# Performance work log

Hardware: AMD Instinct MI355X
Metric: run time of the kernel (lower is better)

## Reference

```python
import jax, jax.numpy as jnp
import numpy as np

HIDDEN = 1024
N_HEADS = 16
HEAD_DIM = HIDDEN // N_HEADS  # 64
SCALE = HEAD_DIM ** -0.5
B, QL, KVL = 2, 2048, 4096


def setup_inputs() -> dict:
    key = jax.random.key(0)
    ks = jax.random.split(key, 7)
    s = 0.02
    return {
        "query_states": jax.random.normal(ks[0], (B, QL, HIDDEN), jnp.float32),
        "key_states": jax.random.normal(ks[1], (B, KVL, HIDDEN), jnp.float32),
        "value_states": jax.random.normal(ks[2], (B, KVL, HIDDEN), jnp.float32),
        # torch nn.Linear weights: shape [out, in], applied as x @ W.T
        "Wq": jax.random.normal(ks[3], (HIDDEN, HIDDEN), jnp.float32) * s,
        "Wk": jax.random.normal(ks[4], (HIDDEN, HIDDEN), jnp.float32) * s,
        "Wv": jax.random.normal(ks[5], (HIDDEN, HIDDEN), jnp.float32) * s,
        "Wo": jax.random.normal(ks[6], (HIDDEN, HIDDEN), jnp.float32) * s,
    }


def reference(query_states, key_states, value_states, Wq, Wk, Wv, Wo):
    b, ql, _ = query_states.shape
    kvl = key_states.shape[1]
    # projections (torch Linear: x @ W.T)
    q = query_states @ Wq.T  # [b, ql, H]
    k = key_states @ Wk.T    # [b, kvl, H]
    v = value_states @ Wv.T  # [b, kvl, H]
    # split heads -> [b, h, s, d]
    q = q.reshape(b, ql, N_HEADS, HEAD_DIM).transpose(0, 2, 1, 3)
    k = k.reshape(b, kvl, N_HEADS, HEAD_DIM).transpose(0, 2, 1, 3)
    v = v.reshape(b, kvl, N_HEADS, HEAD_DIM).transpose(0, 2, 1, 3)
    # scores [b, h, ql, kvl]
    scores = jnp.einsum("bhqd,bhkd->bhqk", q, k) * SCALE
    attn = jax.nn.softmax(scores, axis=-1)
    out = jnp.einsum("bhqk,bhkd->bhqd", attn, v)  # [b, h, ql, d]
    out = out.transpose(0, 2, 1, 3).reshape(b, ql, HIDDEN)
    return out @ Wo.T
```

## Files before the change

### kernel.cpp

```cpp
#include <hip/hip_runtime.h>

#define HID   1024
#define NH    16
#define HD    64
#define QL    2048
#define KVL   4096
#define NB    2
#define QSCALE 0.180336880111120426f

typedef short s8v  __attribute__((ext_vector_type(8)));
typedef short s4v  __attribute__((ext_vector_type(4)));
typedef float f4v  __attribute__((ext_vector_type(4)));

__device__ __forceinline__ unsigned short f2bf(float f) {
  unsigned int u = __builtin_bit_cast(unsigned int, f);
  u += 0x7FFFu + ((u >> 16) & 1u);
  return (unsigned short)(u >> 16);
}
__device__ __forceinline__ float bf2f(unsigned short h) {
  unsigned int u = ((unsigned int)h) << 16;
  return __builtin_bit_cast(float, u);
}
__device__ __forceinline__ float fexp2(float x) {
#if __has_builtin(__builtin_amdgcn_exp2f)
  return __builtin_amdgcn_exp2f(x);
#else
  return exp2f(x);
#endif
}

__global__ __launch_bounds__(256)
void cast_all(const float* __restrict__ q, const float* __restrict__ k,
              const float* __restrict__ v, const float* __restrict__ wq,
              const float* __restrict__ wk, const float* __restrict__ wv,
              const float* __restrict__ wo, unsigned short* __restrict__ dst) {
  size_t c = (size_t)blockIdx.x * 256 + threadIdx.x;
  const float* src; size_t lc; float sc = 1.0f;
  if (c < 524288)       { src = q;  lc = c; }
  else if (c < 1572864) { src = k;  lc = c - 524288; }
  else if (c < 2621440) { src = v;  lc = c - 1572864; }
  else if (c < 2752512) { src = wq; lc = c - 2621440; sc = QSCALE; }
  else if (c < 2883584) { src = wk; lc = c - 2752512; }
  else if (c < 3014656) { src = wv; lc = c - 2883584; }
  else                  { src = wo; lc = c - 3014656; }
  const float4* p = (const float4*)(src + lc * 8);
  float4 a = p[0], b = p[1];
  union { s8v v8; unsigned short h[8]; } u;
  u.h[0] = f2bf(a.x * sc); u.h[1] = f2bf(a.y * sc);
  u.h[2] = f2bf(a.z * sc); u.h[3] = f2bf(a.w * sc);
  u.h[4] = f2bf(b.x * sc); u.h[5] = f2bf(b.y * sc);
  u.h[6] = f2bf(b.z * sc); u.h[7] = f2bf(b.w * sc);
  *(s8v*)(dst + c * 8) = u.v8;
}

typedef const __attribute__((address_space(1))) unsigned int* gas_t;
typedef __attribute__((address_space(3))) unsigned int*       las_t;

__device__ __forceinline__ void gl_lds16(const unsigned short* g, unsigned short* l) {
  __builtin_amdgcn_global_load_lds((gas_t)(const void*)g, (las_t)(void*)l, 16, 0, 0);
}

template <bool OUT_BF16>
__device__ __forceinline__ void gemm_body(const unsigned short* __restrict__ A,
                                          const unsigned short* __restrict__ B,
                                          void* __restrict__ Cv, int N, int K,
                                          int bx, int by,
                                          unsigned short (*As)[128 * 32],
                                          unsigned short (*Bs)[128 * 32]) {
  const int tid  = threadIdx.x;
  const int wave = tid >> 6, lane = tid & 63;
  const int wm = wave >> 1, wn = wave & 1;
  const int quad = lane >> 4, l15 = lane & 15;
  const int row0 = by * 128;
  const int col0 = bx * 128;
  const int srow = lane >> 2;
  const int scol = (lane & 3) * 8;

  f4v acc[4][4] = {};

#define G_STAGE(KI, BI)                                                         \
  {                                                                             \
    _Pragma("unroll")                                                           \
    for (int cc = 0; cc < 2; cc++) {                                            \
      int c = wave + cc * 4;                                                    \
      gl_lds16(A + (size_t)(row0 + c * 16 + srow) * K + (KI) * 32 + scol,       \
               &As[BI][c * 512]);                                               \
      gl_lds16(B + (size_t)(col0 + c * 16 + srow) * K + (KI) * 32 + scol,       \
               &Bs[BI][c * 512]);                                               \
    }                                                                           \
  }

  const int nk = K >> 5;
  G_STAGE(0, 0);
  __syncthreads();

  for (int ki = 0; ki < nk; ki++) {
    const int cur = ki & 1;
    if (ki + 1 < nk) G_STAGE(ki + 1, 1 - cur);

    s8v af[4], bf[4];
#pragma unroll
    for (int i = 0; i < 4; i++)
      af[i] = *(const s8v*)&As[cur][(wm * 64 + i * 16 + l15) * 32 + quad * 8];
#pragma unroll
    for (int j = 0; j < 4; j++)
      bf[j] = *(const s8v*)&Bs[cur][(wn * 64 + j * 16 + l15) * 32 + quad * 8];
#pragma unroll
    for (int i = 0; i < 4; i++)
#pragma unroll
      for (int j = 0; j < 4; j++)
        acc[i][j] = __builtin_amdgcn_mfma_f32_16x16x32_bf16(af[i], bf[j],
                                                            acc[i][j], 0, 0, 0);
    __syncthreads();
  }
#undef G_STAGE

#pragma unroll
  for (int i = 0; i < 4; i++) {
#pragma unroll
    for (int j = 0; j < 4; j++) {
      int r = row0 + wm * 64 + i * 16 + quad * 4;
      int c = col0 + wn * 64 + j * 16 + l15;
#pragma unroll
      for (int reg = 0; reg < 4; reg++) {
        float v = acc[i][j][reg];
        if constexpr (OUT_BF16)
          ((unsigned short*)Cv)[(size_t)(r + reg) * N + c] = f2bf(v);
        else
          ((float*)Cv)[(size_t)(r + reg) * N + c] = v;
      }
    }
  }
}

__global__ __launch_bounds__(256, 4)
void proj_fused(const unsigned short* __restrict__ qc, const unsigned short* __restrict__ kc,
                const unsigned short* __restrict__ vc, const unsigned short* __restrict__ wqc,
                const unsigned short* __restrict__ wkc, const unsigned short* __restrict__ wvc,
                unsigned short* __restrict__ qp, unsigned short* __restrict__ kp,
                unsigned short* __restrict__ vpt) {
  __shared__ unsigned short As[2][128 * 32];
  __shared__ unsigned short Bs[2][128 * 32];
  int bid = blockIdx.x;
  if (bid < 256) {
    gemm_body<true>(qc, wqc, qp, HID, HID, bid & 7, bid >> 3, As, Bs);
  } else if (bid < 768) {
    int l = bid - 256;
    gemm_body<true>(kc, wkc, kp, HID, HID, l & 7, l >> 3, As, Bs);
  } else {
    int l = bid - 768;
    int b = l >> 8, r = l & 255;
    gemm_body<true>(wvc, vc + (size_t)b * KVL * HID,
                    vpt + (size_t)b * HID * KVL, KVL, HID, r & 31, r >> 5, As, Bs);
  }
}

__global__ __launch_bounds__(256, 4)
void o_gemm(const unsigned short* __restrict__ ao, const unsigned short* __restrict__ woc,
            float* __restrict__ out) {
  __shared__ unsigned short As[2][128 * 32];
  __shared__ unsigned short Bs[2][128 * 32];
  int bid = blockIdx.x;
  gemm_body<false>(ao, woc, out, HID, HID, bid & 7, bid >> 3, As, Bs);
}

#define LDSK 40

template <typename T>
__device__ __forceinline__ void stage_tile(unsigned short* dst, const T* src,
                                           int ld, int tid, float sc) {
#pragma unroll
  for (int rep = 0; rep < 2; rep++) {
    int s = rep * 256 + tid;
    int row = s >> 2;
    int cs  = (s & 3) * 8;
    const T* p = src + (size_t)row * ld + cs;
    s8v val;
    if constexpr (sizeof(T) == 4) {
      float4 f0 = *(const float4*)p;
      float4 f1 = *(const float4*)(p + 4);
      union { s8v v; unsigned short h[8]; } u;
      u.h[0] = f2bf(f0.x * sc); u.h[1] = f2bf(f0.y * sc);
      u.h[2] = f2bf(f0.z * sc); u.h[3] = f2bf(f0.w * sc);
      u.h[4] = f2bf(f1.x * sc); u.h[5] = f2bf(f1.y * sc);
      u.h[6] = f2bf(f1.z * sc); u.h[7] = f2bf(f1.w * sc);
      val = u.v;
    } else {
      val = *(const s8v*)p;
    }
    *(s8v*)&dst[row * LDSK + cs] = val;
  }
}

template <typename TA, typename TB, bool OUT_BF16>
__global__ __launch_bounds__(256)
void gemm_conv(const TA* __restrict__ A, const TB* __restrict__ B,
               void* __restrict__ Cv, int M, int N, int K, float bscale,
               long long bz, long long cz) {
  __shared__ unsigned short As[128 * LDSK];
  __shared__ unsigned short Bs[128 * LDSK];
  const TB* Bp = B + (size_t)blockIdx.z * (size_t)bz;
  const int tid  = threadIdx.x;
  const int wave = tid >> 6, lane = tid & 63;
  const int wm = wave >> 1, wn = wave & 1;
  const int quad = lane >> 4, l15 = lane & 15;
  const int row0 = blockIdx.y * 128;
  const int col0 = blockIdx.x * 128;

  f4v acc[4][4] = {};

  for (int k0 = 0; k0 < K; k0 += 32) {
    __syncthreads();
    stage_tile(As, A + (size_t)row0 * K + k0, K, tid, 1.0f);
    stage_tile(Bs, Bp + (size_t)col0 * K + k0, K, tid, bscale);
    __syncthreads();

    s8v af[4], bf[4];
#pragma unroll
    for (int i = 0; i < 4; i++)
      af[i] = *(const s8v*)&As[(wm * 64 + i * 16 + l15) * LDSK + quad * 8];
#pragma unroll
    for (int j = 0; j < 4; j++)
      bf[j] = *(const s8v*)&Bs[(wn * 64 + j * 16 + l15) * LDSK + quad * 8];
#pragma unroll
    for (int i = 0; i < 4; i++)
#pragma unroll
      for (int j = 0; j < 4; j++)
        acc[i][j] = __builtin_amdgcn_mfma_f32_16x16x32_bf16(af[i], bf[j],
                                                            acc[i][j], 0, 0, 0);
  }

  char* Cp = (char*)Cv + (size_t)blockIdx.z * (size_t)cz * (OUT_BF16 ? 2 : 4);
#pragma unroll
  for (int i = 0; i < 4; i++) {
#pragma unroll
    for (int j = 0; j < 4; j++) {
      int r = row0 + wm * 64 + i * 16 + quad * 4;
      int c = col0 + wn * 64 + j * 16 + l15;
#pragma unroll
      for (int reg = 0; reg < 4; reg++) {
        float v = acc[i][j][reg];
        if constexpr (OUT_BF16)
          ((unsigned short*)Cp)[(size_t)(r + reg) * N + c] = f2bf(v);
        else
          ((float*)Cp)[(size_t)(r + reg) * N + c] = v;
      }
    }
  }
}

template <bool SPLIT>
__global__ __launch_bounds__(256, 2)
void attn6(const unsigned short* __restrict__ qp,
           const unsigned short* __restrict__ kp,
           const unsigned short* __restrict__ vpt,
           unsigned short* __restrict__ po,
           float* __restrict__ pl,
           unsigned short* __restrict__ ao) {
  __shared__ unsigned short Ks[2][64 * 64];
  __shared__ unsigned short Vt[2][64 * 64];
  __shared__ unsigned short Pt[4][64 * 64];

  const int bid  = blockIdx.x;
  const int qb   = bid & 7;
  const int h    = (bid >> 3) & 15;
  const int b    = (bid >> 7) & 1;
  const int half = SPLIT ? (bid >> 8) : 0;
  const int tid  = threadIdx.x;
  const int wave = tid >> 6, lane = tid & 63;
  const int quad = lane >> 4, l15 = lane & 15;
  const int q0   = qb * 256 + wave * 64;
  const int kvoff = half * (KVL / 2);
  const int NT   = SPLIT ? (KVL / 128) : (KVL / 64);

  const unsigned short* kbase = kp + (size_t)b * KVL * HID + h * HD + (size_t)kvoff * HID;
  const unsigned short* vbase = vpt + (size_t)(b * NH + h) * HD * KVL + kvoff;

  int prow[2], pcol[2], pbase[2];
#pragma unroll
  for (int i = 0; i < 2; i++) {
    int p = (i * 4 + wave) * 64 + lane;
    prow[i]  = p >> 3;
    pcol[i]  = ((p & 7) ^ (prow[i] & 7)) * 8;
    pbase[i] = (i * 4 + wave) * 512;
  }

  s8v qf[4][2];
#pragma unroll
  for (int nt = 0; nt < 4; nt++) {
    const size_t qrow = (size_t)(b * QL + q0 + nt * 16 + l15) * HID + h * HD;
#pragma unroll
    for (int ks = 0; ks < 2; ks++)
      qf[nt][ks] = *(const s8v*)(qp + qrow + ks * 32 + quad * 8);
  }

  float lrun[4] = {0.f, 0.f, 0.f, 0.f};
  f4v oacc[4][4] = {};

#define STAGE_KV(KT, BI)                                                        \
  {                                                                             \
    const unsigned short* kb = kbase + (size_t)((KT) * 64) * HID;               \
    const unsigned short* vb = vbase + (KT) * 64;                               \
    _Pragma("unroll")                                                           \
    for (int i = 0; i < 2; i++) {                                               \
      gl_lds16(kb + (size_t)prow[i] * HID + pcol[i], &Ks[BI][pbase[i]]);        \
      gl_lds16(vb + (size_t)prow[i] * KVL + pcol[i], &Vt[BI][pbase[i]]);        \
    }                                                                           \
  }

  STAGE_KV(0, 0);
  __syncthreads();

  for (int kt = 0; kt < NT; kt++) {
    const int cur = kt & 1;
    if (kt + 1 < NT) STAGE_KV(kt + 1, 1 - cur);

    f4v sacc[4][4] = {};
#pragma unroll
    for (int ks = 0; ks < 2; ks++)
#pragma unroll
      for (int mt = 0; mt < 4; mt++) {
        int row = mt * 16 + l15;
        int xc  = ((ks * 4 + quad) ^ (row & 7)) * 8;
        s8v kf = *(const s8v*)&Ks[cur][row * 64 + xc];
#pragma unroll
        for (int nt = 0; nt < 4; nt++)
          sacc[mt][nt] = __builtin_amdgcn_mfma_f32_16x16x32_bf16(kf, qf[nt][ks],
                                                                 sacc[mt][nt], 0, 0, 0);
      }

#pragma unroll
    for (int nt = 0; nt < 4; nt++) {
      float rs = 0.f;
#pragma unroll
      for (int mt = 0; mt < 4; mt++) {
        float p0 = fexp2(sacc[mt][nt][0]);
        float p1 = fexp2(sacc[mt][nt][1]);
        float p2 = fexp2(sacc[mt][nt][2]);
        float p3 = fexp2(sacc[mt][nt][3]);
        rs += (p0 + p1) + (p2 + p3);
        union { s4v v4; unsigned short hh[4]; } pk;
        pk.hh[0] = (unsigned short)(__builtin_bit_cast(unsigned int, p0) >> 16);
        pk.hh[1] = (unsigned short)(__builtin_bit_cast(unsigned int, p1) >> 16);
        pk.hh[2] = (unsigned short)(__builtin_bit_cast(unsigned int, p2) >> 16);
        pk.hh[3] = (unsigned short)(__builtin_bit_cast(unsigned int, p3) >> 16);
        int row = nt * 16 + l15;
        int c   = mt * 2 + (quad >> 1);
        int off = ((c ^ (row & 7)) * 8) + (quad & 1) * 4;
        *(s4v*)&Pt[wave][row * 64 + off] = pk.v4;
      }
      rs += __shfl_xor(rs, 16, 64);
      rs += __shfl_xor(rs, 32, 64);
      lrun[nt] += rs;
    }

#pragma unroll
    for (int ch = 0; ch < 2; ch++) {
      s8v vf[4];
#pragma unroll
      for (int dt = 0; dt < 4; dt++) {
        int row = dt * 16 + l15;
        int xc  = ((ch * 4 + quad) ^ (row & 7)) * 8;
        vf[dt] = *(const s8v*)&Vt[cur][row * 64 + xc];
      }
#pragma unroll
      for (int qt = 0; qt < 4; qt++) {
        int row = qt * 16 + l15;
        int xc  = ((ch * 4 + quad) ^ (row & 7)) * 8;
        s8v pf = *(const s8v*)&Pt[wave][row * 64 + xc];
#pragma unroll
        for (int dt = 0; dt < 4; dt++)
          oacc[qt][dt] = __builtin_amdgcn_mfma_f32_16x16x32_bf16(pf, vf[dt],
                                                                 oacc[qt][dt], 0, 0, 0);
      }
    }

    __syncthreads();
  }
#undef STAGE_KV

  if constexpr (SPLIT) {
    unsigned short* pob = po + (size_t)half * NB * QL * HID;
#pragma unroll
    for (int qt = 0; qt < 4; qt++) {
#pragma unroll
      for (int dt = 0; dt < 4; dt++)
#pragma unroll
        for (int r = 0; r < 4; r++) {
          int qq = q0 + qt * 16 + quad * 4 + r;
          int cc = h * HD + dt * 16 + l15;
          pob[(size_t)(b * QL + qq) * HID + cc] = f2bf(oacc[qt][dt][r]);
        }
      if (quad == 0)
        pl[(size_t)half * NB * NH * QL + (b * NH + h) * QL + q0 + qt * 16 + l15] = lrun[qt];
    }
  } else {
#pragma unroll
    for (int qt = 0; qt < 4; qt++) {
      float li = 1.0f / lrun[qt];
      float lr[4];
#pragma unroll
      for (int r = 0; r < 4; r++)
        lr[r] = __shfl(li, (lane & 48) + quad * 4 + r, 64);
#pragma unroll
      for (int dt = 0; dt < 4; dt++)
#pragma unroll
        for (int r = 0; r < 4; r++) {
          int qq = q0 + qt * 16 + quad * 4 + r;
          int cc = h * HD + dt * 16 + l15;
          ao[(size_t)(b * QL + qq) * HID + cc] = f2bf(oacc[qt][dt][r] * lr[r]);
        }
    }
  }
}

__global__ __launch_bounds__(256)
void combine(const unsigned short* __restrict__ po, const float* __restrict__ pl,
             unsigned short* __restrict__ ao) {
  int t  = blockIdx.x * 256 + threadIdx.x;
  int r  = t >> 7;
  int c8 = t & 127;
  int b = r >> 11, q = r & 2047, h = c8 >> 3;
  size_t lidx = (size_t)(b * NH + h) * QL + q;
  float l = pl[lidx] + pl[(size_t)NB * NH * QL + lidx];
  float inv = 1.0f / l;
  size_t off = (size_t)r * HID + c8 * 8;
  s8v a = *(const s8v*)(po + off);
  s8v c = *(const s8v*)(po + (size_t)NB * QL * HID + off);
  union { s8v v8; unsigned short hh[8]; } ua, uc, uo;
  ua.v8 = a; uc.v8 = c;
#pragma unroll
  for (int e = 0; e < 8; e++)
    uo.hh[e] = f2bf((bf2f(ua.hh[e]) + bf2f(uc.hh[e])) * inv);
  *(s8v*)(ao + off) = uo.v8;
}

extern "C" void kernel_launch(void* const* d_in, const int* in_sizes, int n_in,
                              void* d_out, int out_size, void* d_ws, size_t ws_size,
                              hipStream_t stream) {
  const float* q  = (const float*)d_in[0];
  const float* k  = (const float*)d_in[1];
  const float* v  = (const float*)d_in[2];
  const float* Wq = (const float*)d_in[3];
  const float* Wk = (const float*)d_in[4];
  const float* Wv = (const float*)d_in[5];
  const float* Wo = (const float*)d_in[6];
  float* out = (float*)d_out;
  char* ws = (char*)d_ws;
  dim3 blk(256);

  const long long MB = 1024 * 1024;
  if (ws_size >= (size_t)88 * MB) {
    unsigned short* qc  = (unsigned short*)(ws);
    unsigned short* kc  = (unsigned short*)(ws + 8 * MB);
    unsigned short* vc  = (unsigned short*)(ws + 24 * MB);
    unsigned short* wqc = (unsigned short*)(ws + 40 * MB);
    unsigned short* wkc = (unsigned short*)(ws + 42 * MB);
    unsigned short* wvc = (unsigned short*)(ws + 44 * MB);
    unsigned short* woc = (unsigned short*)(ws + 46 * MB);
    unsigned short* qp  = (unsigned short*)(ws + 48 * MB);
    unsigned short* kp  = (unsigned short*)(ws + 56 * MB);
    unsigned short* vpt = (unsigned short*)(ws + 72 * MB);
    unsigned short* ao  = (unsigned short*)(ws);
    unsigned short* po  = (unsigned short*)(ws + 8 * MB);
    float*          pl  = (float*)(ws + 40 * MB);

    cast_all<<<12288, blk, 0, stream>>>(q, k, v, Wq, Wk, Wv, Wo, (unsigned short*)ws);
    proj_fused<<<1280, blk, 0, stream>>>(qc, kc, vc, wqc, wkc, wvc, qp, kp, vpt);
    attn6<true><<<512, blk, 0, stream>>>(qp, kp, vpt, po, pl, nullptr);
    combine<<<2048, blk, 0, stream>>>(po, pl, ao);
    o_gemm<<<256, blk, 0, stream>>>(ao, woc, out);
  } else {
    unsigned short* qp  = (unsigned short*)(ws);
    unsigned short* kp  = (unsigned short*)(ws + 8 * MB);
    unsigned short* vpt = (unsigned short*)(ws + 24 * MB);
    unsigned short* ao  = (unsigned short*)(ws + 40 * MB);

    gemm_conv<float, float, true><<<dim3(8, 32), blk, 0, stream>>>(q, Wq, qp, NB * QL, HID, HID, QSCALE, 0, 0);
    gemm_conv<float, float, true><<<dim3(8, 64), blk, 0, stream>>>(k, Wk, kp, NB * KVL, HID, HID, 1.0f, 0, 0);
    gemm_conv<float, float, true><<<dim3(32, 8, 2), blk, 0, stream>>>(Wv, v, vpt, HID, KVL, HID, 1.0f,
                                                                      (long long)KVL * HID, (long long)HID * KVL);
    attn6<false><<<256, blk, 0, stream>>>(qp, kp, vpt, nullptr, nullptr, ao);
    gemm_conv<unsigned short, float, false><<<dim3(8, 32), blk, 0, stream>>>(ao, Wo, out, NB * QL, HID, HID, 1.0f, 0, 0);
  }
}
```

Measured before the change: 309.0 us.

## Deepen GEMM K-tile to 64 with swizzled LDS and chunk attention P tiles

The projection and output GEMMs now stage 64-wide K slices with an XOR-swizzled LDS layout. This halves the number of barrier iterations and avoids bank conflicts, at the cost of doubling LDS per block and lowering the occupancy hint to 2. The attention kernel processes each 64-key tile in two 32-key chunks, computing scores, exponentials and the PV MFMAs per chunk. This halves the per-wave P buffer and the score accumulator registers, which lets the occupancy hint rise to 3 blocks per CU. The trade-off in attention is less independent MFMA work per chunk between the LDS writes and reads.

```diff
diff --git a/kernel.cpp b/kernel.cpp
--- a/kernel.cpp
+++ b/kernel.cpp
@@ -65,32 +65,38 @@
                                           const unsigned short* __restrict__ B,
                                           void* __restrict__ Cv, int N, int K,
                                           int bx, int by,
-                                          unsigned short (*As)[128 * 32],
-                                          unsigned short (*Bs)[128 * 32]) {
+                                          unsigned short (*As)[128 * 64],
+                                          unsigned short (*Bs)[128 * 64]) {
   const int tid  = threadIdx.x;
   const int wave = tid >> 6, lane = tid & 63;
   const int wm = wave >> 1, wn = wave & 1;
   const int quad = lane >> 4, l15 = lane & 15;
   const int row0 = by * 128;
   const int col0 = bx * 128;
-  const int srow = lane >> 2;
-  const int scol = (lane & 3) * 8;
+
+  int srow[4], scol[4], sbase[4];
+#pragma unroll
+  for (int i = 0; i < 4; i++) {
+    int p = (i * 4 + wave) * 64 + lane;
+    srow[i]  = p >> 3;
+    scol[i]  = ((p & 7) ^ (srow[i] & 7)) * 8;
+    sbase[i] = (i * 4 + wave) * 512;
+  }
 
   f4v acc[4][4] = {};
 
 #define G_STAGE(KI, BI)                                                         \
   {                                                                             \
     _Pragma("unroll")                                                           \
-    for (int cc = 0; cc < 2; cc++) {                                            \
-      int c = wave + cc * 4;                                                    \
-      gl_lds16(A + (size_t)(row0 + c * 16 + srow) * K + (KI) * 32 + scol,       \
-               &As[BI][c * 512]);                                               \
-      gl_lds16(B + (size_t)(col0 + c * 16 + srow) * K + (KI) * 32 + scol,       \
-               &Bs[BI][c * 512]);                                               \
+    for (int i = 0; i < 4; i++) {                                               \
+      gl_lds16(A + (size_t)(row0 + srow[i]) * K + (KI) * 64 + scol[i],          \
+               &As[BI][sbase[i]]);                                              \
+      gl_lds16(B + (size_t)(col0 + srow[i]) * K + (KI) * 64 + scol[i],          \
+               &Bs[BI][sbase[i]]);                                              \
     }                                                                           \
   }
 
-  const int nk = K >> 5;
+  const int nk = K >> 6;
   G_STAGE(0, 0);
   __syncthreads();
 
@@ -98,19 +104,26 @@
     const int cur = ki & 1;
     if (ki + 1 < nk) G_STAGE(ki + 1, 1 - cur);
 
-    s8v af[4], bf[4];
-#pragma unroll
-    for (int i = 0; i < 4; i++)
-      af[i] = *(const s8v*)&As[cur][(wm * 64 + i * 16 + l15) * 32 + quad * 8];
-#pragma unroll
-    for (int j = 0; j < 4; j++)
-      bf[j] = *(const s8v*)&Bs[cur][(wn * 64 + j * 16 + l15) * 32 + quad * 8];
-#pragma unroll
-    for (int i = 0; i < 4; i++)
-#pragma unroll
-      for (int j = 0; j < 4; j++)
-        acc[i][j] = __builtin_amdgcn_mfma_f32_16x16x32_bf16(af[i], bf[j],
-                                                            acc[i][j], 0, 0, 0);
+#pragma unroll
+    for (int ks = 0; ks < 2; ks++) {
+      s8v af[4], bf[4];
+#pragma unroll
+      for (int i = 0; i < 4; i++) {
+        int row = wm * 64 + i * 16 + l15;
+        af[i] = *(const s8v*)&As[cur][row * 64 + ((ks * 4 + quad) ^ (row & 7)) * 8];
+      }
+#pragma unroll
+      for (int j = 0; j < 4; j++) {
+        int row = wn * 64 + j * 16 + l15;
+        bf[j] = *(const s8v*)&Bs[cur][row * 64 + ((ks * 4 + quad) ^ (row & 7)) * 8];
+      }
+#pragma unroll
+      for (int i = 0; i < 4; i++)
+#pragma unroll
+        for (int j = 0; j < 4; j++)
+          acc[i][j] = __builtin_amdgcn_mfma_f32_16x16x32_bf16(af[i], bf[j],
+                                                              acc[i][j], 0, 0, 0);
+    }
     __syncthreads();
   }
 #undef G_STAGE
@@ -133,14 +146,14 @@
   }
 }
 
-__global__ __launch_bounds__(256, 4)
+__global__ __launch_bounds__(256, 2)
 void proj_fused(const unsigned short* __restrict__ qc, const unsigned short* __restrict__ kc,
                 const unsigned short* __restrict__ vc, const unsigned short* __restrict__ wqc,
                 const unsigned short* __restrict__ wkc, const unsigned short* __restrict__ wvc,
                 unsigned short* __restrict__ qp, unsigned short* __restrict__ kp,
                 unsigned short* __restrict__ vpt) {
-  __shared__ unsigned short As[2][128 * 32];
-  __shared__ unsigned short Bs[2][128 * 32];
+  __shared__ unsigned short As[2][128 * 64];
+  __shared__ unsigned short Bs[2][128 * 64];
   int bid = blockIdx.x;
   if (bid < 256) {
     gemm_body<true>(qc, wqc, qp, HID, HID, bid & 7, bid >> 3, As, Bs);
@@ -155,11 +168,11 @@
   }
 }
 
-__global__ __launch_bounds__(256, 4)
+__global__ __launch_bounds__(256, 2)
 void o_gemm(const unsigned short* __restrict__ ao, const unsigned short* __restrict__ woc,
             float* __restrict__ out) {
-  __shared__ unsigned short As[2][128 * 32];
-  __shared__ unsigned short Bs[2][128 * 32];
+  __shared__ unsigned short As[2][128 * 64];
+  __shared__ unsigned short Bs[2][128 * 64];
   int bid = blockIdx.x;
   gemm_body<false>(ao, woc, out, HID, HID, bid & 7, bid >> 3, As, Bs);
 }
@@ -250,8 +263,8 @@
 }
 
 template <bool SPLIT>
-__global__ __launch_bounds__(256, 2)
-void attn6(const unsigned short* __restrict__ qp,
+__global__ __launch_bounds__(256, 3)
+void attn7(const unsigned short* __restrict__ qp,
            const unsigned short* __restrict__ kp,
            const unsigned short* __restrict__ vpt,
            unsigned short* __restrict__ po,
@@ -259,7 +272,7 @@
            unsigned short* __restrict__ ao) {
   __shared__ unsigned short Ks[2][64 * 64];
   __shared__ unsigned short Vt[2][64 * 64];
-  __shared__ unsigned short Pt[4][64 * 64];
+  __shared__ unsigned short Pt[4][64 * 32];
 
   const int bid  = blockIdx.x;
   const int qb   = bid & 7;
@@ -315,64 +328,65 @@
     const int cur = kt & 1;
     if (kt + 1 < NT) STAGE_KV(kt + 1, 1 - cur);
 
-    f4v sacc[4][4] = {};
-#pragma unroll
-    for (int ks = 0; ks < 2; ks++)
-#pragma unroll
-      for (int mt = 0; mt < 4; mt++) {
-        int row = mt * 16 + l15;
-        int xc  = ((ks * 4 + quad) ^ (row & 7)) * 8;
-        s8v kf = *(const s8v*)&Ks[cur][row * 64 + xc];
-#pragma unroll
-        for (int nt = 0; nt < 4; nt++)
-          sacc[mt][nt] = __builtin_amdgcn_mfma_f32_16x16x32_bf16(kf, qf[nt][ks],
-                                                                 sacc[mt][nt], 0, 0, 0);
-      }
-
-#pragma unroll
-    for (int nt = 0; nt < 4; nt++) {
-      float rs = 0.f;
-#pragma unroll
-      for (int mt = 0; mt < 4; mt++) {
-        float p0 = fexp2(sacc[mt][nt][0]);
-        float p1 = fexp2(sacc[mt][nt][1]);
-        float p2 = fexp2(sacc[mt][nt][2]);
-        float p3 = fexp2(sacc[mt][nt][3]);
-        rs += (p0 + p1) + (p2 + p3);
-        union { s4v v4; unsigned short hh[4]; } pk;
-        pk.hh[0] = (unsigned short)(__builtin_bit_cast(unsigned int, p0) >> 16);
-        pk.hh[1] = (unsigned short)(__builtin_bit_cast(unsigned int, p1) >> 16);
-        pk.hh[2] = (unsigned short)(__builtin_bit_cast(unsigned int, p2) >> 16);
-        pk.hh[3] = (unsigned short)(__builtin_bit_cast(unsigned int, p3) >> 16);
+    float rs[4] = {0.f, 0.f, 0.f, 0.f};
+#pragma unroll
+    for (int ch = 0; ch < 2; ch++) {
+      f4v sacc[2][4] = {};
+#pragma unroll
+      for (int ks = 0; ks < 2; ks++)
+#pragma unroll
+        for (int mh = 0; mh < 2; mh++) {
+          int row = (ch * 2 + mh) * 16 + l15;
+          s8v kf = *(const s8v*)&Ks[cur][row * 64 + ((ks * 4 + quad) ^ (row & 7)) * 8];
+#pragma unroll
+          for (int nt = 0; nt < 4; nt++)
+            sacc[mh][nt] = __builtin_amdgcn_mfma_f32_16x16x32_bf16(kf, qf[nt][ks],
+                                                                   sacc[mh][nt], 0, 0, 0);
+        }
+
+#pragma unroll
+      for (int nt = 0; nt < 4; nt++) {
         int row = nt * 16 + l15;
-        int c   = mt * 2 + (quad >> 1);
-        int off = ((c ^ (row & 7)) * 8) + (quad & 1) * 4;
-        *(s4v*)&Pt[wave][row * 64 + off] = pk.v4;
-      }
-      rs += __shfl_xor(rs, 16, 64);
-      rs += __shfl_xor(rs, 32, 64);
-      lrun[nt] += rs;
-    }
-
-#pragma unroll
-    for (int ch = 0; ch < 2; ch++) {
+#pragma unroll
+        for (int mh = 0; mh < 2; mh++) {
+          float p0 = fexp2(sacc[mh][nt][0]);
+          float p1 = fexp2(sacc[mh][nt][1]);
+          float p2 = fexp2(sacc[mh][nt][2]);
+          float p3 = fexp2(sacc[mh][nt][3]);
+          rs[nt] += (p0 + p1) + (p2 + p3);
+          union { s4v v4; unsigned short hh[4]; } pk;
+          pk.hh[0] = (unsigned short)(__builtin_bit_cast(unsigned int, p0) >> 16);
+          pk.hh[1] = (unsigned short)(__builtin_bit_cast(unsigned int, p1) >> 16);
+          pk.hh[2] = (unsigned short)(__builtin_bit_cast(unsigned int, p2) >> 16);
+          pk.hh[3] = (unsigned short)(__builtin_bit_cast(unsigned int, p3) >> 16);
+          int kvi = mh * 16 + quad * 4;
+          int off = ((kvi >> 3) ^ (row & 3)) * 8 + (kvi & 7);
+          *(s4v*)&Pt[wave][row * 32 + off] = pk.v4;
+        }
+      }
+
       s8v vf[4];
 #pragma unroll
       for (int dt = 0; dt < 4; dt++) {
         int row = dt * 16 + l15;
-        int xc  = ((ch * 4 + quad) ^ (row & 7)) * 8;
-        vf[dt] = *(const s8v*)&Vt[cur][row * 64 + xc];
+        vf[dt] = *(const s8v*)&Vt[cur][row * 64 + ((ch * 4 + quad) ^ (row & 7)) * 8];
       }
 #pragma unroll
       for (int qt = 0; qt < 4; qt++) {
         int row = qt * 16 + l15;
-        int xc  = ((ch * 4 + quad) ^ (row & 7)) * 8;
-        s8v pf = *(const s8v*)&Pt[wave][row * 64 + xc];
+        s8v pf = *(const s8v*)&Pt[wave][row * 32 + ((quad ^ (row & 3)) * 8)];
 #pragma unroll
         for (int dt = 0; dt < 4; dt++)
           oacc[qt][dt] = __builtin_amdgcn_mfma_f32_16x16x32_bf16(pf, vf[dt],
                                                                  oacc[qt][dt], 0, 0, 0);
       }
+    }
+
+#pragma unroll
+    for (int nt = 0; nt < 4; nt++) {
+      rs[nt] += __shfl_xor(rs[nt], 16, 64);
+      rs[nt] += __shfl_xor(rs[nt], 32, 64);
+      lrun[nt] += rs[nt];
     }
 
     __syncthreads();
@@ -467,7 +481,7 @@
 
     cast_all<<<12288, blk, 0, stream>>>(q, k, v, Wq, Wk, Wv, Wo, (unsigned short*)ws);
     proj_fused<<<1280, blk, 0, stream>>>(qc, kc, vc, wqc, wkc, wvc, qp, kp, vpt);
-    attn6<true><<<512, blk, 0, stream>>>(qp, kp, vpt, po, pl, nullptr);
+    attn7<true><<<512, blk, 0, stream>>>(qp, kp, vpt, po, pl, nullptr);
     combine<<<2048, blk, 0, stream>>>(po, pl, ao);
     o_gemm<<<256, blk, 0, stream>>>(ao, woc, out);
   } else {
@@ -480,7 +494,7 @@
     gemm_conv<float, float, true><<<dim3(8, 64), blk, 0, stream>>>(k, Wk, kp, NB * KVL, HID, HID, 1.0f, 0, 0);
     gemm_conv<float, float, true><<<dim3(32, 8, 2), blk, 0, stream>>>(Wv, v, vpt, HID, KVL, HID, 1.0f,
                                                                       (long long)KVL * HID, (long long)HID * KVL);
-    attn6<false><<<256, blk, 0, stream>>>(qp, kp, vpt, nullptr, nullptr, ao);
+    attn7<false><<<256, blk, 0, stream>>>(qp, kp, vpt, nullptr, nullptr, ao);
     gemm_conv<unsigned short, float, false><<<dim3(8, 32), blk, 0, stream>>>(ao, Wo, out, NB * QL, HID, HID, 1.0f, 0, 0);
   }
 }
```

Result: slower. 437.9 us (+41.7%).
